# Optimization experiments

Measured on AMD Instinct MI355X. Metric: run time of the kernel, lower is better.

## Reference

```python
import jax, jax.numpy as jnp
import numpy as np

B, T_PREFIX, C_IN = 8, 6144, 8
OUT_LEN, OUT_C = 2048, 8
AUX_DIM = 16
D_MODEL, D_STATE, HEADDIM, EXPAND = 256, 32, 64, 2
D_INNER = EXPAND * D_MODEL            # 512
NHEADS = D_INNER // HEADDIM           # 8
CONV_DIM = D_INNER + 2 * D_STATE      # 576
D_PROJ = 2 * D_INNER + 2 * D_STATE + NHEADS  # 1096
N_LAYERS = 2
CHUNK = 64
PATCH = 16
PRECONV_K = 5
DCONV_K = 4


def setup_inputs() -> dict:
    key = jax.random.key(0)
    ks = iter(jax.random.split(key, 64))
    def rn(shape, s=0.02):
        return s * jax.random.normal(next(ks), shape, jnp.float32)
    inp = dict(
        x_prefix=jax.random.normal(next(ks), (B, T_PREFIX, C_IN), jnp.float32),
        y_aux=jax.random.normal(next(ks), (B, AUX_DIM), jnp.float32),
        pre_conv_w=rn((D_MODEL, C_IN, PRECONV_K), 0.1),
        pre_conv_b=rn((D_MODEL,)),
        patch_w=rn((D_MODEL, D_MODEL, PATCH), 0.05),
        patch_b=rn((D_MODEL,)),
        mask_token=rn((D_MODEL,)),
        aux_w=rn((AUX_DIM, D_MODEL), 0.1),
        aux_b=rn((D_MODEL,)),
        patch_out_w=rn((2 * D_MODEL, OUT_C * PATCH), 0.05),
        patch_out_b=rn((OUT_C * PATCH,)),
    )
    for d in ('fwd', 'bwd'):
        inp[f'{d}_norm_w'] = jnp.ones((N_LAYERS, D_MODEL), jnp.float32)
        inp[f'{d}_inproj'] = rn((N_LAYERS, D_MODEL, D_PROJ), 0.05)
        inp[f'{d}_conv_w'] = rn((N_LAYERS, CONV_DIM, DCONV_K), 0.2)
        inp[f'{d}_conv_b'] = rn((N_LAYERS, CONV_DIM))
        inp[f'{d}_dtbias'] = rn((N_LAYERS, NHEADS), 0.5)
        inp[f'{d}_Alog'] = jnp.tile(jnp.log(jnp.arange(1, NHEADS + 1, dtype=jnp.float32)), (N_LAYERS, 1))
        inp[f'{d}_D'] = jnp.ones((N_LAYERS, NHEADS), jnp.float32)
        inp[f'{d}_gnorm'] = jnp.ones((N_LAYERS, D_INNER), jnp.float32)
        inp[f'{d}_outproj'] = rn((N_LAYERS, D_INNER, D_MODEL), 0.05)
    return inp


def rmsnorm(x, w, eps=1e-5):
    return x * jax.lax.rsqrt(jnp.mean(x * x, axis=-1, keepdims=True) + eps) * w


def conv1d(x, w, b, stride, pad):  # x: [B,C,T], w: [O,I,K]
    y = jax.lax.conv_general_dilated(x, w, (stride,), [(pad, pad)],
                                     dimension_numbers=('NCH', 'OIH', 'NCH'))
    return y + b[None, :, None]


def mamba_block(u, inproj, conv_w, conv_b, dtbias, Alog, Dp, gnorm_w, outproj):
    # Mamba-2/SSD style block: in_proj -> z | xBC | dt, causal depthwise conv,
    # selective scan with per-head scalar decay A, +D skip, gated RMSNorm, out_proj.
    b, T, _ = u.shape
    zxbcdt = u @ inproj                                   # [b,T,D_PROJ]
    z = zxbcdt[..., :D_INNER]
    xBC = zxbcdt[..., D_INNER:D_INNER + CONV_DIM]
    dt = jax.nn.softplus(zxbcdt[..., -NHEADS:] + dtbias)  # [b,T,H]
    # causal depthwise conv over time
    xc = jax.lax.conv_general_dilated(xBC.transpose(0, 2, 1), conv_w[:, None, :], (1,),
                                      [(DCONV_K - 1, 0)],
                                      dimension_numbers=('NCH', 'OIH', 'NCH'),
                                      feature_group_count=CONV_DIM)
    xBC = jax.nn.silu((xc + conv_b[None, :, None]).transpose(0, 2, 1))
    xs = xBC[..., :D_INNER].reshape(b, T, NHEADS, HEADDIM)  # [b,T,H,P]
    Bm = xBC[..., D_INNER:D_INNER + D_STATE]                # [b,T,N]
    Cm = xBC[..., D_INNER + D_STATE:]                       # [b,T,N]
    A = -jnp.exp(Alog)                                      # [H]

    def step(h, inps):  # h: [b,H,P,N]
        dt_t, x_t, B_t, C_t = inps
        dA = jnp.exp(dt_t * A)[:, :, None, None]
        h = h * dA + (dt_t[:, :, None] * x_t)[..., None] * B_t[:, None, None, :]
        y = jnp.einsum('bhpn,bn->bhp', h, C_t)
        return h, y

    h0 = jnp.zeros((b, NHEADS, HEADDIM, D_STATE), u.dtype)
    _, ys = jax.lax.scan(step, h0, (dt.transpose(1, 0, 2), xs.transpose(1, 0, 2, 3),
                                    Bm.transpose(1, 0, 2), Cm.transpose(1, 0, 2)))
    y = ys.transpose(1, 0, 2, 3) + Dp[None, None, :, None] * xs
    y = y.reshape(b, T, D_INNER)
    y = rmsnorm(y * jax.nn.silu(z), gnorm_w)
    return y @ outproj


def reference(x_prefix, y_aux, pre_conv_w, pre_conv_b, patch_w, patch_b, mask_token,
              aux_w, aux_b, fwd_norm_w, fwd_inproj, fwd_conv_w, fwd_conv_b, fwd_dtbias,
              fwd_Alog, fwd_D, fwd_gnorm, fwd_outproj, bwd_norm_w, bwd_inproj,
              bwd_conv_w, bwd_conv_b, bwd_dtbias, bwd_Alog, bwd_D, bwd_gnorm,
              bwd_outproj, patch_out_w, patch_out_b):
    b = x_prefix.shape[0]
    t_total = T_PREFIX + OUT_LEN
    x_full = jnp.pad(x_prefix, ((0, 0), (0, OUT_LEN), (0, 0)))        # zeros for future
    x = jax.nn.silu(conv1d(x_full.transpose(0, 2, 1), pre_conv_w, pre_conv_b, 1, PRECONV_K // 2))
    x = conv1d(x, patch_w, patch_b, PATCH, 0).transpose(0, 2, 1)      # [b, n_tokens, d_model]
    n_tokens = x.shape[1]
    # eval mode: deterministic future-patch mask, dropout is identity
    starts = jnp.arange(n_tokens) * PATCH
    mask = (starts >= T_PREFIX)[None, :, None]
    x = jnp.where(mask, mask_token[None, None, :], x)
    aux_bias = jax.nn.silu(y_aux @ aux_w + aux_b)[:, None, :]
    x = x + aux_bias
    pad_t = (-n_tokens) % CHUNK
    if pad_t:
        x = jnp.pad(x, ((0, 0), (0, pad_t), (0, 0)))
    h_f = x
    h_b = x[:, ::-1]
    for i in range(N_LAYERS):
        h_f = h_f + mamba_block(rmsnorm(h_f, fwd_norm_w[i]), fwd_inproj[i], fwd_conv_w[i],
                                fwd_conv_b[i], fwd_dtbias[i], fwd_Alog[i], fwd_D[i],
                                fwd_gnorm[i], fwd_outproj[i])
        h_b = h_b + mamba_block(rmsnorm(h_b, bwd_norm_w[i]), bwd_inproj[i], bwd_conv_w[i],
                                bwd_conv_b[i], bwd_dtbias[i], bwd_Alog[i], bwd_D[i],
                                bwd_gnorm[i], bwd_outproj[i])
    h = jnp.concatenate([h_f, h_b[:, ::-1]], axis=-1)[:, :n_tokens]   # [b,n,2*d_model]
    patch_pred = h @ patch_out_w + patch_out_b                        # [b,n,out_c*patch]
    y = patch_pred.reshape(b, n_tokens, OUT_C, PATCH).reshape(b, n_tokens * PATCH, OUT_C)
    y = y[:, :t_total, :]
    return y[:, T_PREFIX:, :]
```

## Files before the change

kernel.cpp:

```cpp
#include <hip/hip_runtime.h>
#include <hip/hip_bf16.h>
#include <math.h>

#define BSZ      8
#define TPREF    6144
#define CIN      8
#define DMODEL   256
#define DINNER   512
#define DSTATE   32
#define NHEADS   8
#define HEADDIM  64
#define CONVDIM  576
#define DPROJ    1096
#define ZXW      1088
#define NTOK     512
#define NVIS     384
#define TBWD     128
#define MFWD     (BSZ * NTOK)
#define MBWD     (BSZ * TBWD)
#define MALL     (MFWD + MBWD)

typedef float f32x4 __attribute__((ext_vector_type(4)));
typedef __bf16 bf16x8 __attribute__((ext_vector_type(8)));

__device__ __forceinline__ float silu_f(float x) { return x / (1.f + expf(-x)); }

#define ASYNC16(gp, lp) \
    __builtin_amdgcn_global_load_lds((const __attribute__((address_space(1))) void*)(gp), \
                                     (__attribute__((address_space(3))) void*)(lp), 16, 0, 0)

__global__ __launch_bounds__(256) void gemm_mfma(
    const __bf16* __restrict__ A, const __bf16* __restrict__ Bt,
    float* __restrict__ C, const float* __restrict__ bias,
    int N, int K, int ldc, int flags) {
    __shared__ char sm[16384];
    int tid = threadIdx.x;
    int m0 = blockIdx.y * 128, n0 = blockIdx.x * 128;
    int klen = K / gridDim.z;
    int kbeg = blockIdx.z * klen;
    int w = tid >> 6, l = tid & 63;
    int wm = w >> 1, wn = w & 1;
    int lm = l & 15, q = l >> 4;

    f32x4 acc[4][4];
    #pragma unroll
    for (int i = 0; i < 4; i++)
        #pragma unroll
        for (int j = 0; j < 4; j++) acc[i][j] = (f32x4)0.f;

    for (int k0 = 0; k0 < klen; k0 += 32) {
        int kb = kbeg + k0;
        #pragma unroll
        for (int i = 0; i < 2; i++) {
            int s = i * 256 + tid;
            ASYNC16(A + (size_t)(m0 + (s >> 2)) * K + kb + (s & 3) * 8, sm + s * 16);
        }
        #pragma unroll
        for (int i = 0; i < 2; i++) {
            int s = i * 256 + tid;
            ASYNC16(Bt + (size_t)(n0 + (s >> 2)) * K + kb + (s & 3) * 8, sm + 8192 + s * 16);
        }
        __syncthreads();
        bf16x8 af[4], bfr[4];
        #pragma unroll
        for (int mf = 0; mf < 4; mf++)
            af[mf] = *(const bf16x8*)(sm + (wm * 64 + mf * 16 + lm) * 64 + q * 16);
        #pragma unroll
        for (int nf = 0; nf < 4; nf++)
            bfr[nf] = *(const bf16x8*)(sm + 8192 + (wn * 64 + nf * 16 + lm) * 64 + q * 16);
        #pragma unroll
        for (int mf = 0; mf < 4; mf++)
            #pragma unroll
            for (int nf = 0; nf < 4; nf++)
                acc[mf][nf] = __builtin_amdgcn_mfma_f32_16x16x32_bf16(af[mf], bfr[nf], acc[mf][nf], 0, 0, 0);
        __syncthreads();
    }

    #pragma unroll
    for (int mf = 0; mf < 4; mf++) {
        int mbase = m0 + wm * 64 + mf * 16 + q * 4;
        #pragma unroll
        for (int nf = 0; nf < 4; nf++) {
            int n = n0 + wn * 64 + nf * 16 + lm;
            if (n < N) {
                #pragma unroll
                for (int r = 0; r < 4; r++) {
                    float v = acc[mf][nf][r];
                    if (flags & 4) {
                        v = silu_f(v + bias[n]);
                        ((__bf16*)C)[(size_t)(mbase + r) * ldc + n] = (__bf16)v;
                    } else if (flags & 16) {
                        int mm = mbase + r;
                        int bb = mm / NVIS, tk = mm - bb * NVIS;
                        atomicAdd(C + ((size_t)(bb * NTOK + tk)) * 256 + n, v);
                    } else if (flags & 2) {
                        atomicAdd(C + (size_t)(mbase + r) * ldc + n, v);
                    } else {
                        C[(size_t)(mbase + r) * ldc + n] = v;
                    }
                }
            }
        }
    }
}

__global__ __launch_bounds__(256) void preconv_gemm(
    const float* __restrict__ xp, const __bf16* __restrict__ WpreT,
    const float* __restrict__ bias, __bf16* __restrict__ Apatch) {
    __shared__ char sm[32768];
    int tid = threadIdx.x;
    int m0 = blockIdx.y * 128, n0 = blockIdx.x * 128;
    int w = tid >> 6, l = tid & 63;
    int wm = w >> 1, wn = w & 1, lm = l & 15, q = l >> 4;

    #pragma unroll
    for (int i = 0; i < 4; i++) {
        int s = i * 256 + tid;
        int kh = s >> 9, row = (s & 511) >> 2, within = s & 3;
        ASYNC16(WpreT + (size_t)(n0 + row) * 64 + kh * 32 + within * 8, sm + 16384 + s * 16);
    }
    if (tid < 128) {
        int m = m0 + tid;
        int b = m / TPREF, t = m - b * TPREF;
        __bf16 d[64];
        #pragma unroll
        for (int j = 40; j < 64; j++) d[j] = (__bf16)0.f;
        #pragma unroll
        for (int k = 0; k < 5; k++) {
            int tt = t - 2 + k;
            bool ok = (tt >= 0) && (tt < TPREF);
            const float* s = xp + ((size_t)b * TPREF + tt) * 8;
            #pragma unroll
            for (int i = 0; i < 8; i++)
                d[i * 5 + k] = ok ? (__bf16)s[i] : (__bf16)0.f;
        }
        uint4* o0 = (uint4*)(sm + tid * 64);
        uint4* o1 = (uint4*)(sm + 8192 + tid * 64);
        #pragma unroll
        for (int k = 0; k < 4; k++) { o0[k] = ((const uint4*)d)[k]; o1[k] = ((const uint4*)d)[4 + k]; }
    }
    __syncthreads();

    f32x4 acc[4][4];
    #pragma unroll
    for (int i = 0; i < 4; i++)
        #pragma unroll
        for (int j = 0; j < 4; j++) acc[i][j] = (f32x4)0.f;
    #pragma unroll
    for (int kh = 0; kh < 2; kh++) {
        bf16x8 af[4], bfr[4];
        #pragma unroll
        for (int mf = 0; mf < 4; mf++)
            af[mf] = *(const bf16x8*)(sm + kh * 8192 + (wm * 64 + mf * 16 + lm) * 64 + q * 16);
        #pragma unroll
        for (int nf = 0; nf < 4; nf++)
            bfr[nf] = *(const bf16x8*)(sm + 16384 + kh * 8192 + (wn * 64 + nf * 16 + lm) * 64 + q * 16);
        #pragma unroll
        for (int mf = 0; mf < 4; mf++)
            #pragma unroll
            for (int nf = 0; nf < 4; nf++)
                acc[mf][nf] = __builtin_amdgcn_mfma_f32_16x16x32_bf16(af[mf], bfr[nf], acc[mf][nf], 0, 0, 0);
    }
    #pragma unroll
    for (int mf = 0; mf < 4; mf++) {
        int mbase = m0 + wm * 64 + mf * 16 + q * 4;
        #pragma unroll
        for (int nf = 0; nf < 4; nf++) {
            int n = n0 + wn * 64 + nf * 16 + lm;
            #pragma unroll
            for (int r = 0; r < 4; r++) {
                float v = silu_f(acc[mf][nf][r] + bias[n]);
                Apatch[(size_t)(mbase + r) * 256 + n] = (__bf16)v;
            }
        }
    }
}

__global__ __launch_bounds__(256) void final_gemm(
    const float* __restrict__ h_all, const __bf16* __restrict__ poT,
    float* __restrict__ out) {
    __shared__ __bf16 Asm_[128][40];
    __shared__ char Bsm[8192];
    int tid = threadIdx.x;
    int m0 = blockIdx.y * 128;
    int z = blockIdx.z;
    int dir = z >> 1, kh = z & 1;
    int koff = kh * 128;
    int w = tid >> 6, l = tid & 63;
    int wm = w >> 1, wn_ = w & 1, lm = l & 15, q = l >> 4;
    f32x4 acc[4][4];
    #pragma unroll
    for (int i = 0; i < 4; i++)
        #pragma unroll
        for (int j = 0; j < 4; j++) acc[i][j] = (f32x4)0.f;

    int r = tid >> 1, half = tid & 1;
    int m = m0 + r;
    int b = m >> 7, jj = m & 127;
    size_t arow = (dir == 0) ? ((size_t)(b * NTOK + NVIS + jj) * 256)
                             : ((size_t)MFWD * 256 + (size_t)(b * TBWD + (TBWD - 1 - jj)) * 256);
    for (int k0 = 0; k0 < 128; k0 += 32) {
        {
            const float4* sp = (const float4*)(h_all + arow + koff + k0 + half * 16);
            float4 v0 = sp[0], v1 = sp[1], v2 = sp[2], v3 = sp[3];
            union { uint4 u; __bf16 hh[8]; } d0, d1;
            d0.hh[0] = (__bf16)v0.x; d0.hh[1] = (__bf16)v0.y; d0.hh[2] = (__bf16)v0.z; d0.hh[3] = (__bf16)v0.w;
            d0.hh[4] = (__bf16)v1.x; d0.hh[5] = (__bf16)v1.y; d0.hh[6] = (__bf16)v1.z; d0.hh[7] = (__bf16)v1.w;
            d1.hh[0] = (__bf16)v2.x; d1.hh[1] = (__bf16)v2.y; d1.hh[2] = (__bf16)v2.z; d1.hh[3] = (__bf16)v2.w;
            d1.hh[4] = (__bf16)v3.x; d1.hh[5] = (__bf16)v3.y; d1.hh[6] = (__bf16)v3.z; d1.hh[7] = (__bf16)v3.w;
            *(uint4*)&Asm_[r][half * 16] = d0.u;
            *(uint4*)&Asm_[r][half * 16 + 8] = d1.u;
        }
        #pragma unroll
        for (int i = 0; i < 2; i++) {
            int s = i * 256 + tid;
            ASYNC16(poT + (size_t)(s >> 2) * 512 + dir * 256 + koff + k0 + (s & 3) * 8, Bsm + s * 16);
        }
        __syncthreads();
        bf16x8 af[4], bfr[4];
        #pragma unroll
        for (int mf = 0; mf < 4; mf++)
            af[mf] = *(const bf16x8*)&Asm_[wm * 64 + mf * 16 + lm][q * 8];
        #pragma unroll
        for (int nf = 0; nf < 4; nf++)
            bfr[nf] = *(const bf16x8*)(Bsm + (wn_ * 64 + nf * 16 + lm) * 64 + q * 16);
        #pragma unroll
        for (int mf = 0; mf < 4; mf++)
            #pragma unroll
            for (int nf = 0; nf < 4; nf++)
                acc[mf][nf] = __builtin_amdgcn_mfma_f32_16x16x32_bf16(af[mf], bfr[nf], acc[mf][nf], 0, 0, 0);
        __syncthreads();
    }
    #pragma unroll
    for (int mf = 0; mf < 4; mf++) {
        int mbase = m0 + wm * 64 + mf * 16 + q * 4;
        #pragma unroll
        for (int nf = 0; nf < 4; nf++) {
            int n = wn_ * 64 + nf * 16 + lm;
            #pragma unroll
            for (int rr = 0; rr < 4; rr++)
                atomicAdd(out + (size_t)(mbase + rr) * 128 + n, acc[mf][nf][rr]);
        }
    }
}

__global__ __launch_bounds__(256) void gemm_inproj(
    const __bf16* __restrict__ u, const __bf16* __restrict__ ipTf,
    const __bf16* __restrict__ ipTb, __bf16* __restrict__ zxb, float* __restrict__ dtc) {
    __shared__ char sm[16384];
    int tid = threadIdx.x;
    int m0 = blockIdx.y * 128, n0 = blockIdx.x * 128;
    const __bf16* Bt = (m0 >= MFWD) ? ipTb : ipTf;
    int w = tid >> 6, l = tid & 63;
    int wm = w >> 1, wn = w & 1, lm = l & 15, q = l >> 4;
    f32x4 acc[4][4];
    #pragma unroll
    for (int i = 0; i < 4; i++)
        #pragma unroll
        for (int j = 0; j < 4; j++) acc[i][j] = (f32x4)0.f;
    for (int k0 = 0; k0 < 256; k0 += 32) {
        #pragma unroll
        for (int i = 0; i < 2; i++) {
            int s = i * 256 + tid;
            ASYNC16(u + (size_t)(m0 + (s >> 2)) * 256 + k0 + (s & 3) * 8, sm + s * 16);
        }
        #pragma unroll
        for (int i = 0; i < 2; i++) {
            int s = i * 256 + tid;
            ASYNC16(Bt + (size_t)(n0 + (s >> 2)) * 256 + k0 + (s & 3) * 8, sm + 8192 + s * 16);
        }
        __syncthreads();
        bf16x8 af[4], bfr[4];
        #pragma unroll
        for (int mf = 0; mf < 4; mf++)
            af[mf] = *(const bf16x8*)(sm + (wm * 64 + mf * 16 + lm) * 64 + q * 16);
        #pragma unroll
        for (int nf = 0; nf < 4; nf++)
            bfr[nf] = *(const bf16x8*)(sm + 8192 + (wn * 64 + nf * 16 + lm) * 64 + q * 16);
        #pragma unroll
        for (int mf = 0; mf < 4; mf++)
            #pragma unroll
            for (int nf = 0; nf < 4; nf++)
                acc[mf][nf] = __builtin_amdgcn_mfma_f32_16x16x32_bf16(af[mf], bfr[nf], acc[mf][nf], 0, 0, 0);
        __syncthreads();
    }
    #pragma unroll
    for (int mf = 0; mf < 4; mf++) {
        int mbase = m0 + wm * 64 + mf * 16 + q * 4;
        #pragma unroll
        for (int nf = 0; nf < 4; nf++) {
            int n = n0 + wn * 64 + nf * 16 + lm;
            #pragma unroll
            for (int r = 0; r < 4; r++) {
                float v = acc[mf][nf][r];
                if (n < ZXW) zxb[(size_t)(mbase + r) * ZXW + n] = (__bf16)v;
                else if (n < DPROJ) dtc[(size_t)(mbase + r) * 8 + (n - ZXW)] = v;
            }
        }
    }
}

__global__ __launch_bounds__(256) void gemm_outproj(
    const __bf16* __restrict__ y2, const __bf16* __restrict__ opTf,
    const __bf16* __restrict__ opTb, float* __restrict__ C, int layer) {
    __shared__ char sm[16384];
    int tid = threadIdx.x;
    int yb = blockIdx.y;
    int m0 = (layer == 0) ? yb * 128
                          : ((yb < 8) ? (yb * 512 + 384) : (MFWD + (yb - 8) * 128));
    int n0 = blockIdx.x * 128;
    const __bf16* Bt = (m0 >= MFWD) ? opTb : opTf;
    int w = tid >> 6, l = tid & 63;
    int wm = w >> 1, wn = w & 1, lm = l & 15, q = l >> 4;
    f32x4 acc[4][4];
    #pragma unroll
    for (int i = 0; i < 4; i++)
        #pragma unroll
        for (int j = 0; j < 4; j++) acc[i][j] = (f32x4)0.f;
    for (int k0 = 0; k0 < 512; k0 += 32) {
        #pragma unroll
        for (int i = 0; i < 2; i++) {
            int s = i * 256 + tid;
            ASYNC16(y2 + (size_t)(m0 + (s >> 2)) * 512 + k0 + (s & 3) * 8, sm + s * 16);
        }
        #pragma unroll
        for (int i = 0; i < 2; i++) {
            int s = i * 256 + tid;
            ASYNC16(Bt + (size_t)(n0 + (s >> 2)) * 512 + k0 + (s & 3) * 8, sm + 8192 + s * 16);
        }
        __syncthreads();
        bf16x8 af[4], bfr[4];
        #pragma unroll
        for (int mf = 0; mf < 4; mf++)
            af[mf] = *(const bf16x8*)(sm + (wm * 64 + mf * 16 + lm) * 64 + q * 16);
        #pragma unroll
        for (int nf = 0; nf < 4; nf++)
            bfr[nf] = *(const bf16x8*)(sm + 8192 + (wn * 64 + nf * 16 + lm) * 64 + q * 16);
        #pragma unroll
        for (int mf = 0; mf < 4; mf++)
            #pragma unroll
            for (int nf = 0; nf < 4; nf++)
                acc[mf][nf] = __builtin_amdgcn_mfma_f32_16x16x32_bf16(af[mf], bfr[nf], acc[mf][nf], 0, 0, 0);
        __syncthreads();
    }
    #pragma unroll
    for (int mf = 0; mf < 4; mf++) {
        int mbase = m0 + wm * 64 + mf * 16 + q * 4;
        #pragma unroll
        for (int nf = 0; nf < 4; nf++) {
            int n = n0 + wn * 64 + nf * 16 + lm;
            #pragma unroll
            for (int r = 0; r < 4; r++) {
                size_t ci = (size_t)(mbase + r) * DMODEL + n;
                C[ci] += acc[mf][nf][r];
            }
        }
    }
}

__global__ __launch_bounds__(256) void rmsnorm_all(
    const float* __restrict__ h, const float* __restrict__ wf,
    const float* __restrict__ wb, __bf16* __restrict__ u) {
    int row = blockIdx.x * 4 + (threadIdx.x >> 6);
    int lane = threadIdx.x & 63;
    const float* w = (row >= MFWD) ? wb : wf;
    float4 v = ((const float4*)(h + (size_t)row * 256))[lane];
    float ss = v.x * v.x + v.y * v.y + v.z * v.z + v.w * v.w;
    #pragma unroll
    for (int off = 32; off >= 1; off >>= 1) ss += __shfl_xor(ss, off);
    float rs = rsqrtf(ss * (1.f / 256.f) + 1e-5f);
    float4 wv = ((const float4*)w)[lane];
    __bf16 o4[4] = {(__bf16)(v.x * rs * wv.x), (__bf16)(v.y * rs * wv.y),
                    (__bf16)(v.z * rs * wv.z), (__bf16)(v.w * rs * wv.w)};
    *(uint2*)(u + (size_t)row * 256 + lane * 4) = *(uint2*)o4;
}

__global__ __launch_bounds__(256) void gatednorm_all(
    const __bf16* __restrict__ ysD, const __bf16* __restrict__ zxb,
    const float* __restrict__ gwf, const float* __restrict__ gwb,
    __bf16* __restrict__ y2) {
    int row = blockIdx.x * 4 + (threadIdx.x >> 6);
    int lane = threadIdx.x & 63;
    const float* gw = (row >= MFWD) ? gwb : gwf;
    union { uint4 u; __bf16 hh[8]; } yv, zv;
    yv.u = *(const uint4*)(ysD + (size_t)row * 512 + lane * 8);
    zv.u = *(const uint4*)(zxb + (size_t)row * ZXW + lane * 8);
    float g[8];
    #pragma unroll
    for (int j = 0; j < 8; j++) g[j] = (float)yv.hh[j] * silu_f((float)zv.hh[j]);
    float ss = 0.f;
    #pragma unroll
    for (int j = 0; j < 8; j++) ss += g[j] * g[j];
    #pragma unroll
    for (int off = 32; off >= 1; off >>= 1) ss += __shfl_xor(ss, off);
    float rs = rsqrtf(ss * (1.f / 512.f) + 1e-5f);
    const float4* gr = (const float4*)(gw + lane * 8);
    float4 g0 = gr[0], g1 = gr[1];
    union { uint4 u; __bf16 hh[8]; } d;
    d.hh[0] = (__bf16)(g[0] * rs * g0.x); d.hh[1] = (__bf16)(g[1] * rs * g0.y);
    d.hh[2] = (__bf16)(g[2] * rs * g0.z); d.hh[3] = (__bf16)(g[3] * rs * g0.w);
    d.hh[4] = (__bf16)(g[4] * rs * g1.x); d.hh[5] = (__bf16)(g[5] * rs * g1.y);
    d.hh[6] = (__bf16)(g[6] * rs * g1.z); d.hh[7] = (__bf16)(g[7] * rs * g1.w);
    *(uint4*)(y2 + (size_t)row * 512 + lane * 8) = d.u;
}

__global__ void prep_all(const float* __restrict__ pre_conv_w, const float* __restrict__ patch_w,
                         const float* __restrict__ ip0, const float* __restrict__ ip1,
                         const float* __restrict__ op0, const float* __restrict__ op1,
                         const float* __restrict__ pow_, const float* __restrict__ pob,
                         const float* __restrict__ y_aux, const float* __restrict__ aux_w,
                         const float* __restrict__ aux_b,
                         const float* __restrict__ patch_b, const float* __restrict__ mtok,
                         __bf16* __restrict__ WpreT, __bf16* __restrict__ WtT,
                         __bf16* __restrict__ inprojT, __bf16* __restrict__ outprojT,
                         __bf16* __restrict__ poT, float* __restrict__ dout,
                         float* __restrict__ h_all) {
    __shared__ float tile[32][33];
    int bx = blockIdx.x, tid = threadIdx.x;
    int tx = tid & 31, ty = tid >> 5;
    if (bx < 256) {
        int o = bx, c = tid;
        float f[16];
        const float4* s = (const float4*)(patch_w + (size_t)o * 4096 + c * 16);
        #pragma unroll
        for (int j = 0; j < 4; j++) *(float4*)&f[j * 4] = s[j];
        #pragma unroll
        for (int k = 0; k < 16; k++)
            WtT[(size_t)o * 4096 + k * 256 + c] = (__bf16)f[k];
        return;
    }
    bx -= 256;
    if (bx < 1152) {
        int seg = bx / 288, rem = bx % 288;
        int n0 = (rem / 8) * 32, k0 = (rem % 8) * 32;
        const float* src = (seg < 2 ? ip0 : ip1) + (size_t)(seg & 1) * 256 * DPROJ;
        #pragma unroll
        for (int j = 0; j < 4; j++) {
            int r = ty + j * 8;
            int n = n0 + tx;
            tile[r][tx] = (n < DPROJ) ? src[(size_t)(k0 + r) * DPROJ + n] : 0.f;
        }
        __syncthreads();
        __bf16* dst = inprojT + (size_t)seg * 1152 * 256;
        #pragma unroll
        for (int j = 0; j < 4; j++) {
            int r = ty + j * 8;
            dst[(size_t)(n0 + r) * 256 + k0 + tx] = (__bf16)tile[tx][r];
        }
        return;
    }
    bx -= 1152;
    if (bx < 512) {
        int s = bx / 128, rem = bx % 128;
        int n0 = (rem / 16) * 32, k0 = (rem % 16) * 32;
        const float* src = (s < 2 ? op0 : op1) + (size_t)(s & 1) * DINNER * DMODEL;
        #pragma unroll
        for (int j = 0; j < 4; j++) {
            int r = ty + j * 8;
            tile[r][tx] = src[(size_t)(k0 + r) * 256 + n0 + tx];
        }
        __syncthreads();
        __bf16* dst = outprojT + (size_t)s * 256 * 512;
        #pragma unroll
        for (int j = 0; j < 4; j++) {
            int r = ty + j * 8;
            dst[(size_t)(n0 + r) * 512 + k0 + tx] = (__bf16)tile[tx][r];
        }
        return;
    }
    bx -= 512;
    if (bx < 64) {
        int n0 = (bx / 16) * 32, k0 = (bx % 16) * 32;
        #pragma unroll
        for (int j = 0; j < 4; j++) {
            int r = ty + j * 8;
            tile[r][tx] = pow_[(size_t)(k0 + r) * 128 + n0 + tx];
        }
        __syncthreads();
        #pragma unroll
        for (int j = 0; j < 4; j++) {
            int r = ty + j * 8;
            poT[(size_t)(n0 + r) * 512 + k0 + tx] = (__bf16)tile[tx][r];
        }
        return;
    }
    bx -= 64;
    if (bx < 64) {
        int idx = bx * 256 + tid;
        int o = idx >> 6, kk = idx & 63;
        WpreT[idx] = (kk < 40) ? (__bf16)pre_conv_w[o * 40 + kk] : (__bf16)0.f;
        return;
    }
    bx -= 64;
    if (bx < 512) {
        int idx = bx * 256 + tid;
        dout[idx] = pob[idx & 127];
        return;
    }
    bx -= 512;
    {
        int row = bx, o = tid;
        int b; bool masked;
        if (row < MFWD) { b = row >> 9; int tok = row & 511; masked = (tok >= NVIS); }
        else { b = (row - MFWD) >> 7; masked = true; }
        float acc = aux_b[o];
        #pragma unroll
        for (int i = 0; i < 16; i++) acc += y_aux[b * 16 + i] * aux_w[i * 256 + o];
        float v = (masked ? mtok[o] : patch_b[o]) + silu_f(acc);
        h_all[(size_t)row * 256 + o] = v;
    }
}

__global__ __launch_bounds__(256) void dwconv2_kernel(
    const __bf16* __restrict__ zxb, const float* __restrict__ cwf, const float* __restrict__ cbf,
    const float* __restrict__ cwb, const float* __restrict__ cbb,
    __bf16* __restrict__ XtF, __bf16* __restrict__ XtB,
    __bf16* __restrict__ BCF, __bf16* __restrict__ BCB) {
    int cg = blockIdx.x;
    int id = blockIdx.y;
    int b, t0, T; size_t rowbase;
    const float *cw, *cb; __bf16 *Xt, *BC;
    if (id < 64) { b = id >> 3; t0 = (id & 7) * 64; T = NTOK; rowbase = (size_t)b * NTOK;
                   cw = cwf; cb = cbf; Xt = XtF; BC = BCF; }
    else { int i2 = id - 64; b = i2 >> 1; t0 = (i2 & 1) * 64; T = TBWD;
           rowbase = (size_t)MFWD + (size_t)b * TBWD; cw = cwb; cb = cbb; Xt = XtB; BC = BCB; }
    int c0 = cg * 64;
    __shared__ float xs[67][65];
    int lane = threadIdx.x & 63, grp = threadIdx.x >> 6;
    for (int r = grp; r < 67; r += 4) {
        int t = t0 - 3 + r;
        xs[r][lane] = (t >= 0) ? (float)zxb[(rowbase + t) * ZXW + DINNER + c0 + lane] : 0.f;
    }
    __syncthreads();
    if (cg < 8) {
        int t = lane;
        #pragma unroll
        for (int ci = grp; ci < 64; ci += 4) {
            int c = c0 + ci;
            float acc = cb[c];
            #pragma unroll
            for (int k = 0; k < 4; k++) acc += cw[c * 4 + k] * xs[t + k][ci];
            Xt[((size_t)((b * 8 + cg) * 64 + ci)) * T + t0 + t] = (__bf16)silu_f(acc);
        }
    } else {
        int c = lane;
        #pragma unroll
        for (int ti = grp; ti < 64; ti += 4) {
            float acc = cb[c0 + c];
            #pragma unroll
            for (int k = 0; k < 4; k++) acc += cw[(c0 + c) * 4 + k] * xs[ti + k][c];
            BC[((size_t)(b * T + t0 + ti)) * 64 + c] = (__bf16)silu_f(acc);
        }
    }
}

__global__ __launch_bounds__(256) void scan_local(
    const __bf16* __restrict__ XtF, const __bf16* __restrict__ XtB,
    const __bf16* __restrict__ BCF, const __bf16* __restrict__ BCB,
    const float* __restrict__ dtc,
    const float* __restrict__ dtbf, const float* __restrict__ dtbb,
    const float* __restrict__ Alogf, const float* __restrict__ Alogb,
    const float* __restrict__ Dpf, const float* __restrict__ Dpb,
    __bf16* __restrict__ ysD,
    __bf16* __restrict__ ChatF, __bf16* __restrict__ ChatB,
    float* __restrict__ dSF, float* __restrict__ dSB,
    float* __restrict__ DcsF, float* __restrict__ DcsB, int layer) {
    int id = blockIdx.x, hd = blockIdx.y;
    int b, c, T, NC; size_t rowbase;
    const __bf16 *Xt, *BC; __bf16* Chat; float *dS, *Dcs;
    const float *dtb, *Alog, *Dp;
    if (id < 64) { b = id >> 3; c = id & 7; T = NTOK; NC = 8; rowbase = (size_t)b * NTOK;
                   Xt = XtF; BC = BCF; Chat = ChatF; dS = dSF; Dcs = DcsF;
                   dtb = dtbf; Alog = Alogf; Dp = Dpf; }
    else { int i2 = id - 64; b = i2 >> 1; c = i2 & 1; T = TBWD; NC = 2;
           rowbase = (size_t)MFWD + (size_t)b * TBWD;
           Xt = XtB; BC = BCB; Chat = ChatB; dS = dSB; Dcs = DcsB;
           dtb = dtbb; Alog = Alogb; Dp = Dpb; }
    bool skipY = (layer == 1) && (id < 64) && (c < 6);
    int bh = b * 8 + hd;
    int t0 = c * 64;
    int tid = threadIdx.x;
    int w = tid >> 6, l = tid & 63;
    int lm = l & 15, q = l >> 4;
    float A = -expf(Alog[hd]);
    float Dh = Dp[hd];

    __shared__ char smem[23552];
    __bf16 (*Xl)[72]  = (__bf16(*)[72])(smem);
    __bf16 (*BCl)[72] = (__bf16(*)[72])(smem + 9216);
    __bf16 (*Pl)[72]  = (__bf16(*)[72])(smem + 9216);
    __bf16 (*Wbl)[72] = (__bf16(*)[72])(smem + 18432);
    float* lcs = (float*)(smem + 23040);
    float* dts = (float*)(smem + 23296);

    {
        int r = tid >> 2, seg = tid & 3;
        const uint4* xg = (const uint4*)(Xt + (size_t)(bh * 64 + r) * T + t0) + seg * 2;
        uint4 x0 = xg[0], x1 = xg[1];
        const uint4* bg = (const uint4*)(BC + ((size_t)(b * T + t0 + r)) * 64) + seg * 2;
        uint4 b0 = bg[0], b1 = bg[1];
        *(uint4*)&Xl[r][seg * 16]      = x0;
        *(uint4*)&Xl[r][seg * 16 + 8]  = x1;
        *(uint4*)&BCl[r][seg * 16]     = b0;
        *(uint4*)&BCl[r][seg * 16 + 8] = b1;
    }
    float xdt = dtc[(rowbase + t0 + l) * 8 + hd] + dtb[hd];
    float dtv = (xdt > 20.f) ? xdt : log1pf(expf(xdt));
    float lc = A * dtv;
    #pragma unroll
    for (int off = 1; off < 64; off <<= 1) {
        float o = __shfl_up(lc, off);
        if (l >= off) lc += o;
    }
    float lc63 = __shfl(lc, 63);
    float wj = expf(lc63 - lc) * dtv;
    float eli = expf(lc);
    if (w == 0) {
        lcs[l] = lc; dts[l] = dtv;
        if (l == 0) Dcs[bh * NC + c] = expf(lc63);
    }
    __syncthreads();

    if (!skipY) {
        union { uint4 u; __bf16 h[8]; } s, d;
        s.u = *(const uint4*)&BCl[l][32 + w * 8];
        #pragma unroll
        for (int j = 0; j < 8; j++) d.h[j] = (__bf16)(eli * (float)s.h[j]);
        *(uint4*)(Chat + ((size_t)(bh * NC + c) * 64 + l) * 32 + w * 8) = d.u;
    }
    {
        union { uint4 u; __bf16 h[8]; } s;
        s.u = *(const uint4*)&BCl[l][w * 8];
        #pragma unroll
        for (int j = 0; j < 8; j++) Wbl[w * 8 + j][l] = (__bf16)(wj * (float)s.h[j]);
    }
    bf16x8 cfr, bfr[4];
    if (!skipY) {
        cfr = *(const bf16x8*)&BCl[w * 16 + lm][32 + q * 8];
        #pragma unroll
        for (int tj = 0; tj < 4; tj++)
            if (tj <= w) bfr[tj] = *(const bf16x8*)&BCl[tj * 16 + lm][q * 8];
    }
    __syncthreads();

    if (!skipY) {
        float lci[4];
        #pragma unroll
        for (int r = 0; r < 4; r++) lci[r] = lcs[w * 16 + q * 4 + r];
        #pragma unroll
        for (int tj = 0; tj < 4; tj++) {
            if (tj > w) {
                #pragma unroll
                for (int r = 0; r < 4; r++) Pl[w * 16 + q * 4 + r][tj * 16 + lm] = (__bf16)0.f;
                continue;
            }
            f32x4 g = __builtin_amdgcn_mfma_f32_16x16x32_bf16(cfr, bfr[tj], (f32x4)0.f, 0, 0, 0);
            int j = tj * 16 + lm;
            float lcj = lcs[j], dtj = dts[j];
            #pragma unroll
            for (int r = 0; r < 4; r++) {
                int i = w * 16 + q * 4 + r;
                float v = (j <= i) ? g[r] * expf(lci[r] - lcj) * dtj : 0.f;
                if (j == i) v += Dh;
                Pl[i][j] = (__bf16)v;
            }
        }
    }
    __syncthreads();

    bf16x8 xf0[4], xf1[4];
    #pragma unroll
    for (int t4 = 0; t4 < 4; t4++) {
        xf0[t4] = *(const bf16x8*)&Xl[t4 * 16 + lm][q * 8];
        xf1[t4] = *(const bf16x8*)&Xl[t4 * 16 + lm][32 + q * 8];
    }
    if (!skipY) {
        bf16x8 pf0 = *(const bf16x8*)&Pl[w * 16 + lm][q * 8];
        bf16x8 pf1 = *(const bf16x8*)&Pl[w * 16 + lm][32 + q * 8];
        #pragma unroll
        for (int tp = 0; tp < 4; tp++) {
            f32x4 y = __builtin_amdgcn_mfma_f32_16x16x32_bf16(pf0, xf0[tp], (f32x4)0.f, 0, 0, 0);
            y = __builtin_amdgcn_mfma_f32_16x16x32_bf16(pf1, xf1[tp], y, 0, 0, 0);
            #pragma unroll
            for (int r = 0; r < 4; r++) {
                int i = w * 16 + q * 4 + r;
                ysD[(rowbase + t0 + i) * DINNER + hd * 64 + tp * 16 + lm] = (__bf16)y[r];
            }
        }
    }
    bf16x8 wf0[2], wf1[2];
    #pragma unroll
    for (int tn = 0; tn < 2; tn++) {
        wf0[tn] = *(const bf16x8*)&Wbl[tn * 16 + lm][q * 8];
        wf1[tn] = *(const bf16x8*)&Wbl[tn * 16 + lm][32 + q * 8];
    }
    float* dso = dS + (size_t)(bh * NC + c) * 2048;
    #pragma unroll
    for (int tn = 0; tn < 2; tn++) {
        f32x4 s = __builtin_amdgcn_mfma_f32_16x16x32_bf16(xf0[w], wf0[tn], (f32x4)0.f, 0, 0, 0);
        s = __builtin_amdgcn_mfma_f32_16x16x32_bf16(xf1[w], wf1[tn], s, 0, 0, 0);
        #pragma unroll
        for (int r = 0; r < 4; r++) {
            int pp = w * 16 + q * 4 + r, nn = tn * 16 + lm;
            dso[pp * 32 + nn] = s[r];
        }
    }
}

__global__ __launch_bounds__(256) void scan_tail(
    const float* __restrict__ dSF, const float* __restrict__ dSB,
    const float* __restrict__ DcsF, const float* __restrict__ DcsB,
    const __bf16* __restrict__ ChatF, const __bf16* __restrict__ ChatB,
    __bf16* __restrict__ ysD, int layer) {
    int blk = blockIdx.x;
    int dir = blk >= 64;
    int bh = blk & 63;
    int NC = dir ? 2 : 8;
    int T = dir ? TBWD : NTOK;
    int b = bh >> 3, hd = bh & 7;
    size_t rowbase = dir ? ((size_t)MFWD + (size_t)b * TBWD) : ((size_t)b * NTOK);
    const float* dS = dir ? dSB : dSF;
    const float* Dcs = dir ? DcsB : DcsF;
    const __bf16* Chat = dir ? ChatB : ChatF;
    int cmin = (layer == 1 && !dir) ? 6 : 1;
    int tid = threadIdx.x;
    __shared__ __bf16 Spl[8][64][40];
    {
        int p = tid >> 2, n0 = (tid & 3) * 8;
        float S[8];
        #pragma unroll
        for (int j = 0; j < 8; j++) S[j] = 0.f;
        for (int c = 0; c < NC; c++) {
            union { uint4 u; __bf16 hh[8]; } o;
            #pragma unroll
            for (int j = 0; j < 8; j++) o.hh[j] = (__bf16)S[j];
            *(uint4*)&Spl[c][p][n0] = o.u;
            float Dc = Dcs[bh * NC + c];
            const float4* dp = (const float4*)(dS + ((size_t)(bh * NC + c)) * 2048 + tid * 8);
            float4 d0 = dp[0], d1 = dp[1];
            S[0] = Dc * S[0] + d0.x; S[1] = Dc * S[1] + d0.y;
            S[2] = Dc * S[2] + d0.z; S[3] = Dc * S[3] + d0.w;
            S[4] = Dc * S[4] + d1.x; S[5] = Dc * S[5] + d1.y;
            S[6] = Dc * S[6] + d1.z; S[7] = Dc * S[7] + d1.w;
        }
    }
    __syncthreads();
    int w = tid >> 6, l = tid & 63, lm = l & 15, q = l >> 4;
    for (int c = cmin + w; c < NC; c += 4) {
        int t0 = c * 64;
        const __bf16* Cb = Chat + (size_t)(bh * NC + c) * 2048;
        bf16x8 cf[4], sf[4];
        #pragma unroll
        for (int t4 = 0; t4 < 4; t4++) {
            cf[t4] = *(const bf16x8*)(Cb + (t4 * 16 + lm) * 32 + q * 8);
            sf[t4] = *(const bf16x8*)&Spl[c][t4 * 16 + lm][q * 8];
        }
        #pragma unroll
        for (int ti = 0; ti < 4; ti++) {
            #pragma unroll
            for (int tp = 0; tp < 4; tp++) {
                f32x4 y = __builtin_amdgcn_mfma_f32_16x16x32_bf16(cf[ti], sf[tp], (f32x4)0.f, 0, 0, 0);
                #pragma unroll
                for (int r = 0; r < 4; r++) {
                    int i = ti * 16 + q * 4 + r;
                    size_t idx = (rowbase + t0 + i) * DINNER + hd * 64 + tp * 16 + lm;
                    ysD[idx] = (__bf16)((float)ysD[idx] + y[r]);
                }
            }
        }
    }
}

extern "C" void kernel_launch(void* const* d_in, const int* in_sizes, int n_in,
                              void* d_out, int out_size, void* d_ws, size_t ws_size,
                              hipStream_t stream) {
    const float* x_prefix    = (const float*)d_in[0];
    const float* y_aux       = (const float*)d_in[1];
    const float* pre_conv_w  = (const float*)d_in[2];
    const float* pre_conv_b  = (const float*)d_in[3];
    const float* patch_w     = (const float*)d_in[4];
    const float* patch_b     = (const float*)d_in[5];
    const float* mask_token  = (const float*)d_in[6];
    const float* aux_w       = (const float*)d_in[7];
    const float* aux_b       = (const float*)d_in[8];
    const float* patch_out_w = (const float*)d_in[9];
    const float* patch_out_b = (const float*)d_in[10];
    const float* w_norm[2]   = {(const float*)d_in[11], (const float*)d_in[20]};
    const float* w_inproj[2] = {(const float*)d_in[12], (const float*)d_in[21]};
    const float* w_convw[2]  = {(const float*)d_in[13], (const float*)d_in[22]};
    const float* w_convb[2]  = {(const float*)d_in[14], (const float*)d_in[23]};
    const float* w_dtb[2]    = {(const float*)d_in[15], (const float*)d_in[24]};
    const float* w_alog[2]   = {(const float*)d_in[16], (const float*)d_in[25]};
    const float* w_D[2]      = {(const float*)d_in[17], (const float*)d_in[26]};
    const float* w_gnorm[2]  = {(const float*)d_in[18], (const float*)d_in[27]};
    const float* w_outproj[2]= {(const float*)d_in[19], (const float*)d_in[28]};

    char* p = (char*)d_ws;
    auto alloc = [&](size_t bytes) { char* r = p; p += (bytes + 255) & ~255ULL; return r; };
    __bf16* A_patch  = (__bf16*)alloc((size_t)3072 * 4096 * 2);
    __bf16* WpreT    = (__bf16*)alloc((size_t)256 * 64 * 2);
    __bf16* WtT      = (__bf16*)alloc((size_t)256 * 4096 * 2);
    __bf16* inprojT  = (__bf16*)alloc((size_t)4 * 1152 * 256 * 2);
    __bf16* outprojT = (__bf16*)alloc((size_t)4 * 256 * 512 * 2);
    __bf16* poT      = (__bf16*)alloc((size_t)128 * 512 * 2);
    float*  h_all    = (float*)alloc((size_t)MALL * 256 * 4);
    __bf16* u        = (__bf16*)alloc((size_t)MALL * 256 * 2);
    __bf16* zxb      = (__bf16*)alloc((size_t)MALL * ZXW * 2);
    float*  dtc      = (float*)alloc((size_t)MALL * 8 * 4);
    __bf16* XtF      = (__bf16*)alloc((size_t)64 * 64 * NTOK * 2);
    __bf16* XtB      = (__bf16*)alloc((size_t)64 * 64 * TBWD * 2);
    __bf16* BCF      = (__bf16*)alloc((size_t)BSZ * NTOK * 64 * 2);
    __bf16* BCB      = (__bf16*)alloc((size_t)BSZ * TBWD * 64 * 2);
    __bf16* ysD      = (__bf16*)alloc((size_t)MALL * DINNER * 2);
    __bf16* y2       = (__bf16*)alloc((size_t)MALL * DINNER * 2);
    __bf16* ChatF    = (__bf16*)alloc((size_t)64 * 8 * 2048 * 2);
    __bf16* ChatB    = (__bf16*)alloc((size_t)64 * 2 * 2048 * 2);
    float*  dSF      = (float*)alloc((size_t)64 * 8 * 2048 * 4);
    float*  dSB      = (float*)alloc((size_t)64 * 2 * 2048 * 4);
    float*  DcsF     = (float*)alloc((size_t)64 * 8 * 4);
    float*  DcsB     = (float*)alloc((size_t)64 * 2 * 4);

    prep_all<<<256 + 1152 + 512 + 64 + 64 + 512 + MALL, 256, 0, stream>>>(
        pre_conv_w, patch_w, w_inproj[0], w_inproj[1], w_outproj[0], w_outproj[1],
        patch_out_w, patch_out_b, y_aux, aux_w, aux_b, patch_b, mask_token,
        WpreT, WtT, inprojT, outprojT, poT, (float*)d_out, h_all);
    preconv_gemm<<<dim3(2, (BSZ * TPREF) / 128), 256, 0, stream>>>(
        x_prefix, WpreT, pre_conv_b, A_patch);
    gemm_mfma<<<dim3(2, 24, 8), 256, 0, stream>>>(
        A_patch, WtT, h_all, nullptr, 256, 4096, 256, 16);

    for (int i = 0; i < 2; i++) {
        const __bf16* ipTf = inprojT + (size_t)(0 * 2 + i) * 1152 * 256;
        const __bf16* ipTb = inprojT + (size_t)(1 * 2 + i) * 1152 * 256;
        const __bf16* opTf = outprojT + (size_t)(0 * 2 + i) * 256 * 512;
        const __bf16* opTb = outprojT + (size_t)(1 * 2 + i) * 256 * 512;
        rmsnorm_all<<<MALL / 4, 256, 0, stream>>>(h_all, w_norm[0] + i * 256, w_norm[1] + i * 256, u);
        gemm_inproj<<<dim3(9, MALL / 128), 256, 0, stream>>>(u, ipTf, ipTb, zxb, dtc);
        dwconv2_kernel<<<dim3(9, 80), 256, 0, stream>>>(
            zxb, w_convw[0] + i * CONVDIM * 4, w_convb[0] + i * CONVDIM,
            w_convw[1] + i * CONVDIM * 4, w_convb[1] + i * CONVDIM,
            XtF, XtB, BCF, BCB);
        scan_local<<<dim3(80, NHEADS), 256, 0, stream>>>(
            XtF, XtB, BCF, BCB, dtc,
            w_dtb[0] + i * 8, w_dtb[1] + i * 8,
            w_alog[0] + i * 8, w_alog[1] + i * 8,
            w_D[0] + i * 8, w_D[1] + i * 8,
            ysD, ChatF, ChatB, dSF, dSB, DcsF, DcsB, i);
        scan_tail<<<128, 256, 0, stream>>>(dSF, dSB, DcsF, DcsB, ChatF, ChatB, ysD, i);
        gatednorm_all<<<MALL / 4, 256, 0, stream>>>(
            ysD, zxb, w_gnorm[0] + i * DINNER, w_gnorm[1] + i * DINNER, y2);
        int oy = (i == 0) ? (MALL / 128) : 16;
        gemm_outproj<<<dim3(2, oy), 256, 0, stream>>>(y2, opTf, opTb, h_all, i);
    }

    final_gemm<<<dim3(1, 8, 4), 256, 0, stream>>>(h_all, poT, (float*)d_out);
}
```

Before: 328.7 us.

## Fuse depthwise causal conv into scan_local, drop Xt/BC intermediates

Removes the separate dwconv2 kernel and computes the causal depthwise conv plus SiLU inside scan_local. Each block loads raw xBC rows, including a 3-row halo, from zxb into shared memory and writes the transposed X tile and BC tile directly. This removes one launch per layer and the global write/read round trip of XtF/XtB/BCF/BCB. In exchange the BC conv is recomputed by all 8 head blocks, and shared memory per block grows from about 23 KB to about 40 KB, which may lower occupancy.

Measured after the change: 323.3 us. No clear change (-1.6%).

```diff
diff --git a/kernel.cpp b/kernel.cpp
--- a/kernel.cpp
+++ b/kernel.cpp
@@ -511,52 +511,10 @@
     }
 }
 
-__global__ __launch_bounds__(256) void dwconv2_kernel(
-    const __bf16* __restrict__ zxb, const float* __restrict__ cwf, const float* __restrict__ cbf,
+__global__ __launch_bounds__(256) void scan_local(
+    const __bf16* __restrict__ zxb,
+    const float* __restrict__ cwf, const float* __restrict__ cbf,
     const float* __restrict__ cwb, const float* __restrict__ cbb,
-    __bf16* __restrict__ XtF, __bf16* __restrict__ XtB,
-    __bf16* __restrict__ BCF, __bf16* __restrict__ BCB) {
-    int cg = blockIdx.x;
-    int id = blockIdx.y;
-    int b, t0, T; size_t rowbase;
-    const float *cw, *cb; __bf16 *Xt, *BC;
-    if (id < 64) { b = id >> 3; t0 = (id & 7) * 64; T = NTOK; rowbase = (size_t)b * NTOK;
-                   cw = cwf; cb = cbf; Xt = XtF; BC = BCF; }
-    else { int i2 = id - 64; b = i2 >> 1; t0 = (i2 & 1) * 64; T = TBWD;
-           rowbase = (size_t)MFWD + (size_t)b * TBWD; cw = cwb; cb = cbb; Xt = XtB; BC = BCB; }
-    int c0 = cg * 64;
-    __shared__ float xs[67][65];
-    int lane = threadIdx.x & 63, grp = threadIdx.x >> 6;
-    for (int r = grp; r < 67; r += 4) {
-        int t = t0 - 3 + r;
-        xs[r][lane] = (t >= 0) ? (float)zxb[(rowbase + t) * ZXW + DINNER + c0 + lane] : 0.f;
-    }
-    __syncthreads();
-    if (cg < 8) {
-        int t = lane;
-        #pragma unroll
-        for (int ci = grp; ci < 64; ci += 4) {
-            int c = c0 + ci;
-            float acc = cb[c];
-            #pragma unroll
-            for (int k = 0; k < 4; k++) acc += cw[c * 4 + k] * xs[t + k][ci];
-            Xt[((size_t)((b * 8 + cg) * 64 + ci)) * T + t0 + t] = (__bf16)silu_f(acc);
-        }
-    } else {
-        int c = lane;
-        #pragma unroll
-        for (int ti = grp; ti < 64; ti += 4) {
-            float acc = cb[c0 + c];
-            #pragma unroll
-            for (int k = 0; k < 4; k++) acc += cw[(c0 + c) * 4 + k] * xs[ti + k][c];
-            BC[((size_t)(b * T + t0 + ti)) * 64 + c] = (__bf16)silu_f(acc);
-        }
-    }
-}
-
-__global__ __launch_bounds__(256) void scan_local(
-    const __bf16* __restrict__ XtF, const __bf16* __restrict__ XtB,
-    const __bf16* __restrict__ BCF, const __bf16* __restrict__ BCB,
     const float* __restrict__ dtc,
     const float* __restrict__ dtbf, const float* __restrict__ dtbb,
     const float* __restrict__ Alogf, const float* __restrict__ Alogb,
@@ -567,15 +525,15 @@
     float* __restrict__ DcsF, float* __restrict__ DcsB, int layer) {
     int id = blockIdx.x, hd = blockIdx.y;
     int b, c, T, NC; size_t rowbase;
-    const __bf16 *Xt, *BC; __bf16* Chat; float *dS, *Dcs;
-    const float *dtb, *Alog, *Dp;
+    __bf16* Chat; float *dS, *Dcs;
+    const float *dtb, *Alog, *Dp, *cw, *cb;
     if (id < 64) { b = id >> 3; c = id & 7; T = NTOK; NC = 8; rowbase = (size_t)b * NTOK;
-                   Xt = XtF; BC = BCF; Chat = ChatF; dS = dSF; Dcs = DcsF;
-                   dtb = dtbf; Alog = Alogf; Dp = Dpf; }
+                   Chat = ChatF; dS = dSF; Dcs = DcsF;
+                   dtb = dtbf; Alog = Alogf; Dp = Dpf; cw = cwf; cb = cbf; }
     else { int i2 = id - 64; b = i2 >> 1; c = i2 & 1; T = TBWD; NC = 2;
            rowbase = (size_t)MFWD + (size_t)b * TBWD;
-           Xt = XtB; BC = BCB; Chat = ChatB; dS = dSB; Dcs = DcsB;
-           dtb = dtbb; Alog = Alogb; Dp = Dpb; }
+           Chat = ChatB; dS = dSB; Dcs = DcsB;
+           dtb = dtbb; Alog = Alogb; Dp = Dpb; cw = cwb; cb = cbb; }
     bool skipY = (layer == 1) && (id < 64) && (c < 6);
     int bh = b * 8 + hd;
     int t0 = c * 64;
@@ -585,24 +543,62 @@
     float A = -expf(Alog[hd]);
     float Dh = Dp[hd];
 
-    __shared__ char smem[23552];
+    __shared__ char smem[40704];
     __bf16 (*Xl)[72]  = (__bf16(*)[72])(smem);
     __bf16 (*BCl)[72] = (__bf16(*)[72])(smem + 9216);
     __bf16 (*Pl)[72]  = (__bf16(*)[72])(smem + 9216);
     __bf16 (*Wbl)[72] = (__bf16(*)[72])(smem + 18432);
     float* lcs = (float*)(smem + 23040);
     float* dts = (float*)(smem + 23296);
+    __bf16 (*xraw)[64] = (__bf16(*)[64])(smem + 23552);
+    __bf16 (*braw)[64] = (__bf16(*)[64])(smem + 32128);
+
+    for (int s = tid; s < 1072; s += 256) {
+        int arr = (s >= 536) ? 1 : 0;
+        int s2 = s - arr * 536;
+        int r = s2 >> 3, seg = s2 & 7;
+        int t = t0 - 3 + r;
+        uint4 v = make_uint4(0u, 0u, 0u, 0u);
+        if (t >= 0) {
+            size_t col = arr ? (size_t)(1024 + seg * 8) : (size_t)(DINNER + hd * 64 + seg * 8);
+            v = *(const uint4*)(zxb + (rowbase + t) * (size_t)ZXW + col);
+        }
+        if (arr) *(uint4*)&braw[r][seg * 8] = v;
+        else     *(uint4*)&xraw[r][seg * 8] = v;
+    }
+    __syncthreads();
 
     {
-        int r = tid >> 2, seg = tid & 3;
-        const uint4* xg = (const uint4*)(Xt + (size_t)(bh * 64 + r) * T + t0) + seg * 2;
-        uint4 x0 = xg[0], x1 = xg[1];
-        const uint4* bg = (const uint4*)(BC + ((size_t)(b * T + t0 + r)) * 64) + seg * 2;
-        uint4 b0 = bg[0], b1 = bg[1];
-        *(uint4*)&Xl[r][seg * 16]      = x0;
-        *(uint4*)&Xl[r][seg * 16 + 8]  = x1;
-        *(uint4*)&BCl[r][seg * 16]     = b0;
-        *(uint4*)&BCl[r][seg * 16 + 8] = b1;
+        int cX = hd * 64 + l;
+        float w0 = cw[cX * 4], w1 = cw[cX * 4 + 1], w2 = cw[cX * 4 + 2], w3 = cw[cX * 4 + 3];
+        float cbv = cb[cX];
+        int tb = w * 16;
+        float a0 = (float)xraw[tb][l], a1 = (float)xraw[tb + 1][l], a2 = (float)xraw[tb + 2][l];
+        union { uint4 u; __bf16 h[8]; } p0, p1;
+        #pragma unroll
+        for (int j = 0; j < 16; j++) {
+            float a3 = (float)xraw[tb + j + 3][l];
+            float acc = cbv + w0 * a0 + w1 * a1 + w2 * a2 + w3 * a3;
+            if (j < 8) p0.h[j] = (__bf16)silu_f(acc);
+            else       p1.h[j - 8] = (__bf16)silu_f(acc);
+            a0 = a1; a1 = a2; a2 = a3;
+        }
+        *(uint4*)&Xl[l][tb]     = p0.u;
+        *(uint4*)&Xl[l][tb + 8] = p1.u;
+    }
+    {
+        int cc = 512 + l;
+        float w0 = cw[cc * 4], w1 = cw[cc * 4 + 1], w2 = cw[cc * 4 + 2], w3 = cw[cc * 4 + 3];
+        float cbv = cb[cc];
+        int tb = w * 16;
+        float a0 = (float)braw[tb][l], a1 = (float)braw[tb + 1][l], a2 = (float)braw[tb + 2][l];
+        #pragma unroll
+        for (int j = 0; j < 16; j++) {
+            float a3 = (float)braw[tb + j + 3][l];
+            float acc = cbv + w0 * a0 + w1 * a1 + w2 * a2 + w3 * a3;
+            BCl[tb + j][l] = (__bf16)silu_f(acc);
+            a0 = a1; a1 = a2; a2 = a3;
+        }
     }
     float xdt = dtc[(rowbase + t0 + l) * 8 + hd] + dtb[hd];
     float dtv = (xdt > 20.f) ? xdt : log1pf(expf(xdt));
@@ -807,10 +803,6 @@
     __bf16* u        = (__bf16*)alloc((size_t)MALL * 256 * 2);
     __bf16* zxb      = (__bf16*)alloc((size_t)MALL * ZXW * 2);
     float*  dtc      = (float*)alloc((size_t)MALL * 8 * 4);
-    __bf16* XtF      = (__bf16*)alloc((size_t)64 * 64 * NTOK * 2);
-    __bf16* XtB      = (__bf16*)alloc((size_t)64 * 64 * TBWD * 2);
-    __bf16* BCF      = (__bf16*)alloc((size_t)BSZ * NTOK * 64 * 2);
-    __bf16* BCB      = (__bf16*)alloc((size_t)BSZ * TBWD * 64 * 2);
     __bf16* ysD      = (__bf16*)alloc((size_t)MALL * DINNER * 2);
     __bf16* y2       = (__bf16*)alloc((size_t)MALL * DINNER * 2);
     __bf16* ChatF    = (__bf16*)alloc((size_t)64 * 8 * 2048 * 2);
@@ -836,12 +828,11 @@
         const __bf16* opTb = outprojT + (size_t)(1 * 2 + i) * 256 * 512;
         rmsnorm_all<<<MALL / 4, 256, 0, stream>>>(h_all, w_norm[0] + i * 256, w_norm[1] + i * 256, u);
         gemm_inproj<<<dim3(9, MALL / 128), 256, 0, stream>>>(u, ipTf, ipTb, zxb, dtc);
-        dwconv2_kernel<<<dim3(9, 80), 256, 0, stream>>>(
-            zxb, w_convw[0] + i * CONVDIM * 4, w_convb[0] + i * CONVDIM,
+        scan_local<<<dim3(80, NHEADS), 256, 0, stream>>>(
+            zxb,
+            w_convw[0] + i * CONVDIM * 4, w_convb[0] + i * CONVDIM,
             w_convw[1] + i * CONVDIM * 4, w_convb[1] + i * CONVDIM,
-            XtF, XtB, BCF, BCB);
-        scan_local<<<dim3(80, NHEADS), 256, 0, stream>>>(
-            XtF, XtB, BCF, BCB, dtc,
+            dtc,
             w_dtb[0] + i * 8, w_dtb[1] + i * 8,
             w_alog[0] + i * 8, w_alog[1] + i * 8,
             w_D[0] + i * 8, w_D[1] + i * 8,
```
